# Optimization experiments

Measured on AMD Instinct MI355X. Metric: run time of the kernel, lower is better.

## Reference

```python
import jax, jax.numpy as jnp
import numpy as np

D_K = 128
SCALER = np.sqrt(D_K).astype(np.float32)

def setup_inputs() -> dict:
    key = jax.random.key(0)
    kq, kk, kv = jax.random.split(key, 3)
    B, L, D = 16, 2048, D_K
    q = jax.random.normal(kq, (B, L, D), dtype=jnp.float32)
    k = jax.random.normal(kk, (B, L, D), dtype=jnp.float32)
    v = jax.random.normal(kv, (B, L, D), dtype=jnp.float32)
    return {"q": q, "k": k, "v": v}

def reference(q, k, v):
    # score[b, i, j] = q[b, i, :] . k[b, j, :] / sqrt(d_k)
    score = jnp.einsum('bid,bjd->bij', q, k) / SCALER
    attn = jax.nn.softmax(score, axis=-1)
    # output[b, i, :] = sum_j attn[b, i, j] * v[b, j, :]
    return jnp.einsum('bij,bjd->bid', attn, v)
```

## Files before the change

kernel.cpp:

```cpp
#include <hip/hip_runtime.h>
#include <stdint.h>


typedef short bf16x8 __attribute__((ext_vector_type(8)));
typedef float f32x4 __attribute__((ext_vector_type(4)));
typedef float f32x16 __attribute__((ext_vector_type(16)));
typedef unsigned int u32;
typedef unsigned short u16;

#define L_SEQ  2048
#define D_HEAD 128
#define TSZ    8388608u
#define W_PART (2u * TSZ)
#define W_LSUM (W_PART + 512u * 32768u)
#define WS_NEED (W_LSUM + 512u * 128u * 4u)

__device__ __forceinline__ unsigned pk2(float lo, float hi) {
    union { float f; unsigned u; } a, b;
    a.f = lo; b.f = hi;
    return __builtin_amdgcn_perm(b.u + 0x8000u, a.u + 0x8000u, 0x07060302u);
}
__device__ __forceinline__ float ex2(float x) { return __builtin_amdgcn_exp2f(x); }
__device__ __forceinline__ float bflo(unsigned w) {
    union { unsigned u; float f; } v; v.u = w << 16; return v.f;
}
__device__ __forceinline__ float bfhi(unsigned w) {
    union { unsigned u; float f; } v; v.u = w & 0xffff0000u; return v.f;
}
__device__ __forceinline__ u32 cvtpk(float lo, float hi) {
    u32 d;
    asm("v_cvt_pk_bf16_f32 %0, %1, %2" : "=v"(d) : "v"(lo), "v"(hi));
    return d;
}
__device__ __forceinline__ void plswap(u32& a, u32& b) {
    asm volatile("v_permlane32_swap_b32 %0, %1" : "+v"(a), "+v"(b));
}
__device__ __forceinline__ void gl_lds16(const u16* g, u16* l) {
    __builtin_amdgcn_global_load_lds(
        (const __attribute__((address_space(1))) u32*)g,
        (__attribute__((address_space(3))) u32*)l, 16, 0, 0);
}

__global__ __launch_bounds__(256, 4)
void prepass(const float* __restrict__ K, const float* __restrict__ V,
             u16* __restrict__ kb, u16* __restrict__ vt) {
    const int id = blockIdx.x, t = threadIdx.x;
    if (id < 512) {
        const float* src = K + (size_t)id * 64 * 128;
        u16*        dst = kb + (size_t)id * 64 * 128;
        const int r = t >> 2;
        #pragma unroll
        for (int i = 0; i < 4; ++i) {
            int gp = (t & 3) * 4 + i;
            const float* s = src + r * 128 + gp * 8;
            float4 x0 = *(const float4*)s, x1 = *(const float4*)(s + 4);
            uint4 w;
            w.x = pk2(x0.x, x0.y); w.y = pk2(x0.z, x0.w);
            w.z = pk2(x1.x, x1.y); w.w = pk2(x1.z, x1.w);
            *(uint4*)(dst + (gp * 64 + r) * 8) = w;
        }
    } else {
        __shared__ __align__(16) u16 vl[128 * 72];
        const int bid = id - 512;
        const float* src = V + (size_t)bid * 64 * 128;
        const int vcc = t & 31, vgk = t >> 5;
        union { float4 v; float f[4]; } vr[8];
        const float* vp = src + (size_t)(vgk * 8) * 128 + vcc * 4;
        #pragma unroll
        for (int r = 0; r < 8; ++r) vr[r].v = *(const float4*)(vp + (size_t)r * 128);
        #pragma unroll
        for (int dd = 0; dd < 4; ++dd) {
            uint4 w;
            w.x = pk2(vr[0].f[dd], vr[1].f[dd]);
            w.y = pk2(vr[2].f[dd], vr[3].f[dd]);
            w.z = pk2(vr[4].f[dd], vr[5].f[dd]);
            w.w = pk2(vr[6].f[dd], vr[7].f[dd]);
            *(uint4*)(&vl[(vcc * 4 + dd) * 72 + vgk * 8]) = w;
        }
        __syncthreads();
        u16* dst = vt + (size_t)bid * 8192;
        #pragma unroll
        for (int i = 0; i < 4; ++i) {
            int c = i * 256 + t;
            int gv = c >> 7, d = c & 127;
            uint4 w = *(const uint4*)(&vl[d * 72 + gv * 8]);
            *(uint4*)(dst + (size_t)c * 8) = w;
        }
    }
}

__global__ __launch_bounds__(256, 2)
void attnR(const float* __restrict__ Qg, const u16* __restrict__ kb,
           const u16* __restrict__ vt, u16* __restrict__ part,
           float* __restrict__ lsum) {
    __shared__ __align__(16) char smem[32768];
    const int tid = threadIdx.x;
    const int qs = tid >> 6, lane = tid & 63;
    const int q32 = lane & 31, hi = lane >> 5;
    const int bid = blockIdx.x;
    const int kvh = bid >> 8, p = bid & 255;
    const int b = p & 15, qblk = p >> 4;
    const int nt = 16;

    const float* Qp = Qg + (size_t)b * L_SEQ * D_HEAD;
    const u16*   Kp = kb + (size_t)b * L_SEQ * D_HEAD + (size_t)kvh * 16 * 8192;
    const u16*   Vp = vt + (size_t)b * 32 * 8192 + (size_t)kvh * 16 * 8192;
    u16* Kl = (u16*)smem;
    u16* Vl = (u16*)(smem + 16384);
    const int so = qs * 2048 + lane * 8;

    #pragma unroll
    for (int i = 0; i < 4; ++i) {
        gl_lds16(Kp + so + i * 512, Kl + so + i * 512);
        gl_lds16(Vp + so + i * 512, Vl + so + i * 512);
    }

    const float QS = 1.4426950408889634f / 11.313708498984761f;
    bf16x8 qf[8];
    {
        const float* qrow = Qp + (size_t)(qblk * 128 + qs * 32 + q32) * 128 + hi * 8;
        #pragma unroll
        for (int s8 = 0; s8 < 8; ++s8) {
            float4 x0 = *(const float4*)(qrow + s8 * 16);
            float4 x1 = *(const float4*)(qrow + s8 * 16 + 4);
            union { u32 u[4]; bf16x8 v; } tt;
            tt.u[0] = pk2(x0.x * QS, x0.y * QS);
            tt.u[1] = pk2(x0.z * QS, x0.w * QS);
            tt.u[2] = pk2(x1.x * QS, x1.y * QS);
            tt.u[3] = pk2(x1.z * QS, x1.w * QS);
            qf[s8] = tt.v;
        }
    }

    f32x16 acc[4];
    #pragma unroll
    for (int dt = 0; dt < 4; ++dt)
        acc[dt] = (f32x16){0.f,0.f,0.f,0.f,0.f,0.f,0.f,0.f,
                           0.f,0.f,0.f,0.f,0.f,0.f,0.f,0.f};
    float lrun = 0.f;

    __syncthreads();

    for (int it = 0; it < nt; ++it) {
        f32x16 st0 = (f32x16){0.f,0.f,0.f,0.f,0.f,0.f,0.f,0.f,
                              0.f,0.f,0.f,0.f,0.f,0.f,0.f,0.f};
        f32x16 st1 = st0;
        const u16* Kbase = Kl + hi * 512 + q32 * 8;
        __builtin_amdgcn_s_setprio(1);
        #pragma unroll
        for (int s8 = 0; s8 < 8; ++s8) {
            bf16x8 a0 = *(const bf16x8*)(Kbase + s8 * 1024);
            bf16x8 a1 = *(const bf16x8*)(Kbase + s8 * 1024 + 256);
            st0 = __builtin_amdgcn_mfma_f32_32x32x16_bf16(a0, qf[s8], st0, 0, 0, 0);
            st1 = __builtin_amdgcn_mfma_f32_32x32x16_bf16(a1, qf[s8], st1, 0, 0, 0);
        }
        __builtin_amdgcn_s_setprio(0);
        __syncthreads();

        if (it + 1 < nt) {
            const u16* kg = Kp + (size_t)(it + 1) * 8192 + so;
            #pragma unroll
            for (int i = 0; i < 4; ++i) gl_lds16(kg + i * 512, Kl + so + i * 512);
        }

        bf16x8 pf[4];
        #pragma unroll
        for (int v = 0; v < 2; ++v) {
            float pp[16];
            #pragma unroll
            for (int e = 0; e < 16; ++e) {
                float sv = (v == 0) ? st0[e] : st1[e];
                pp[e] = ex2(sv);
                lrun += pp[e];
            }
            u32 wa0 = cvtpk(pp[0], pp[1]),  wb0 = cvtpk(pp[4], pp[5]);
            u32 wa1 = cvtpk(pp[2], pp[3]),  wb1 = cvtpk(pp[6], pp[7]);
            plswap(wa0, wb0); plswap(wa1, wb1);
            u32 wc0 = cvtpk(pp[8], pp[9]),  wd0 = cvtpk(pp[12], pp[13]);
            u32 wc1 = cvtpk(pp[10], pp[11]), wd1 = cvtpk(pp[14], pp[15]);
            plswap(wc0, wd0); plswap(wc1, wd1);
            union { u32 u[4]; bf16x8 x; } t0u, t1u;
            t0u.u[0] = wa0; t0u.u[1] = wa1; t0u.u[2] = wb0; t0u.u[3] = wb1;
            t1u.u[0] = wc0; t1u.u[1] = wc1; t1u.u[2] = wd0; t1u.u[3] = wd1;
            pf[v * 2]     = t0u.x;
            pf[v * 2 + 1] = t1u.x;
        }

        const u16* Vbase = Vl + hi * 1024 + q32 * 8;
        __builtin_amdgcn_s_setprio(1);
        #pragma unroll
        for (int dt = 0; dt < 4; ++dt) {
            #pragma unroll
            for (int ks = 0; ks < 4; ++ks) {
                bf16x8 av = *(const bf16x8*)(Vbase + ks * 2048 + dt * 256);
                acc[dt] = __builtin_amdgcn_mfma_f32_32x32x16_bf16(av, pf[ks], acc[dt], 0, 0, 0);
            }
        }
        __builtin_amdgcn_s_setprio(0);
        __syncthreads();

        if (it + 1 < nt) {
            const u16* vg = Vp + (size_t)(it + 1) * 8192 + so;
            #pragma unroll
            for (int i = 0; i < 4; ++i) gl_lds16(vg + i * 512, Vl + so + i * 512);
        }
    }

    float l = lrun + __shfl_xor(lrun, 32);
    uint2* pw = (uint2*)(part + (size_t)bid * 16384);
    #pragma unroll
    for (int dt = 0; dt < 4; ++dt) {
        f32x16 o = acc[dt];
        #pragma unroll
        for (int jj = 0; jj < 4; ++jj) {
            uint2 w;
            w.x = pk2(o[jj * 4 + 0], o[jj * 4 + 1]);
            w.y = pk2(o[jj * 4 + 2], o[jj * 4 + 3]);
            pw[(((qs * 4 + dt) * 4 + jj) << 6) + lane] = w;
        }
    }
    if (lane < 32)
        lsum[(size_t)bid * 128 + qs * 32 + lane] = l;
}

__global__ __launch_bounds__(256, 2)
void combineR(const u16* __restrict__ part, const float* __restrict__ lsum,
              float* __restrict__ Og) {
    __shared__ float inv[128];
    __shared__ __align__(16) float Ol[64 * 132];
    const int t = threadIdx.x, p = blockIdx.x;
    const int b = p & 15, qblk = p >> 4;
    if (t < 128) {
        float l = lsum[(size_t)p * 128 + t] + lsum[(size_t)(256 + p) * 128 + t];
        inv[t] = 1.0f / l;
    }
    const uint2* S0 = (const uint2*)(part + (size_t)p * 16384);
    const uint2* S1 = (const uint2*)(part + (size_t)(256 + p) * 16384);
    __syncthreads();
    #pragma unroll
    for (int h = 0; h < 2; ++h) {
        #pragma unroll
        for (int i = 0; i < 8; ++i) {
            int slot = i * 256 + t;
            int qs_l = slot >> 10;
            int dt   = (slot >> 8) & 3;
            int jj   = (slot >> 6) & 3;
            int lane = slot & 63;
            int hi = lane >> 5, q32 = lane & 31;
            int qs = h * 2 + qs_l;
            int row_l = qs_l * 32 + q32;
            int d0 = dt * 32 + hi * 4 + jj * 8;
            size_t idx = (size_t)(((qs * 4 + dt) * 4 + jj) << 6) + lane;
            uint2 w0 = S0[idx], w1 = S1[idx];
            float iv = inv[h * 64 + row_l];
            float4 o;
            o.x = (bflo(w0.x) + bflo(w1.x)) * iv;
            o.y = (bfhi(w0.x) + bfhi(w1.x)) * iv;
            o.z = (bflo(w0.y) + bflo(w1.y)) * iv;
            o.w = (bfhi(w0.y) + bfhi(w1.y)) * iv;
            *(float4*)(&Ol[row_l * 132 + d0]) = o;
        }
        __syncthreads();
        #pragma unroll
        for (int i = 0; i < 8; ++i) {
            int slot = i * 256 + t;
            int row = slot >> 5, c4 = slot & 31;
            float4 val = *(const float4*)(&Ol[row * 132 + c4 * 4]);
            size_t q = (size_t)b * L_SEQ + qblk * 128 + h * 64 + row;
            *(float4*)(Og + q * D_HEAD + c4 * 4) = val;
        }
        __syncthreads();
    }
}

extern "C" void kernel_launch(void* const* d_in, const int* in_sizes, int n_in,
                              void* d_out, int out_size, void* d_ws, size_t ws_size,
                              hipStream_t stream) {
    const float* q = (const float*)d_in[0];
    const float* k = (const float*)d_in[1];
    const float* v = (const float*)d_in[2];
    float* out = (float*)d_out;
    u16* kb = (u16*)d_ws;
    u16* vt = (u16*)((char*)d_ws + TSZ);
    u16* part = (u16*)((char*)d_ws + W_PART);
    float* ls = (float*)((char*)d_ws + W_LSUM);
    prepass<<<dim3(1024), dim3(256), 0, stream>>>(k, v, kb, vt);
    attnR<<<dim3(512), dim3(256), 0, stream>>>(q, kb, vt, part, ls);
    combineR<<<dim3(256), dim3(256), 0, stream>>>(part, ls, out);
}
```

Baseline: 134.1 us.

## Fuse split-KV combine into attention kernel via last-arriver atomic flag

Removes the separate combine kernel. Each attention block stores its partial output and row sums, then bumps a per-tile counter; the second block to arrive reads its partner's partial and writes the normalized output directly from its own fp32 accumulators. This saves a kernel launch and a full round trip of partials, and the arriving block's own half stays in fp32 rather than being rounded to bf16. In exchange it relies on agent-scope atomics for cross-block visibility, writes output with uncoalesced per-lane float4 stores without LDS staging, and also drops the s_setprio hints around the MFMA loops.

Result: slower. 146.8 us (+9.5%).

```diff
diff --git a/kernel.cpp b/kernel.cpp
--- a/kernel.cpp
+++ b/kernel.cpp
@@ -3,9 +3,9 @@
 
 
 typedef short bf16x8 __attribute__((ext_vector_type(8)));
-typedef float f32x4 __attribute__((ext_vector_type(4)));
 typedef float f32x16 __attribute__((ext_vector_type(16)));
 typedef unsigned int u32;
+typedef unsigned long long u64;
 typedef unsigned short u16;
 
 #define L_SEQ  2048
@@ -13,7 +13,7 @@
 #define TSZ    8388608u
 #define W_PART (2u * TSZ)
 #define W_LSUM (W_PART + 512u * 32768u)
-#define WS_NEED (W_LSUM + 512u * 128u * 4u)
+#define W_FLAG (W_LSUM + 512u * 128u * 4u)
 
 __device__ __forceinline__ unsigned pk2(float lo, float hi) {
     union { float f; unsigned u; } a, b;
@@ -43,8 +43,10 @@
 
 __global__ __launch_bounds__(256, 4)
 void prepass(const float* __restrict__ K, const float* __restrict__ V,
-             u16* __restrict__ kb, u16* __restrict__ vt) {
+             u16* __restrict__ kb, u16* __restrict__ vt, int* __restrict__ flag) {
     const int id = blockIdx.x, t = threadIdx.x;
+    if (id == 0)
+        __hip_atomic_store(&flag[t], 0, __ATOMIC_RELAXED, __HIP_MEMORY_SCOPE_AGENT);
     if (id < 512) {
         const float* src = K + (size_t)id * 64 * 128;
         u16*        dst = kb + (size_t)id * 64 * 128;
@@ -92,8 +94,10 @@
 __global__ __launch_bounds__(256, 2)
 void attnR(const float* __restrict__ Qg, const u16* __restrict__ kb,
            const u16* __restrict__ vt, u16* __restrict__ part,
-           float* __restrict__ lsum) {
+           float* __restrict__ lsum, int* __restrict__ flag,
+           float* __restrict__ Og) {
     __shared__ __align__(16) char smem[32768];
+    __shared__ int role;
     const int tid = threadIdx.x;
     const int qs = tid >> 6, lane = tid & 63;
     const int q32 = lane & 31, hi = lane >> 5;
@@ -146,7 +150,6 @@
                               0.f,0.f,0.f,0.f,0.f,0.f,0.f,0.f};
         f32x16 st1 = st0;
         const u16* Kbase = Kl + hi * 512 + q32 * 8;
-        __builtin_amdgcn_s_setprio(1);
         #pragma unroll
         for (int s8 = 0; s8 < 8; ++s8) {
             bf16x8 a0 = *(const bf16x8*)(Kbase + s8 * 1024);
@@ -154,7 +157,6 @@
             st0 = __builtin_amdgcn_mfma_f32_32x32x16_bf16(a0, qf[s8], st0, 0, 0, 0);
             st1 = __builtin_amdgcn_mfma_f32_32x32x16_bf16(a1, qf[s8], st1, 0, 0, 0);
         }
-        __builtin_amdgcn_s_setprio(0);
         __syncthreads();
 
         if (it + 1 < nt) {
@@ -187,7 +189,6 @@
         }
 
         const u16* Vbase = Vl + hi * 1024 + q32 * 8;
-        __builtin_amdgcn_s_setprio(1);
         #pragma unroll
         for (int dt = 0; dt < 4; ++dt) {
             #pragma unroll
@@ -196,7 +197,6 @@
                 acc[dt] = __builtin_amdgcn_mfma_f32_32x32x16_bf16(av, pf[ks], acc[dt], 0, 0, 0);
             }
         }
-        __builtin_amdgcn_s_setprio(0);
         __syncthreads();
 
         if (it + 1 < nt) {
@@ -207,69 +207,49 @@
     }
 
     float l = lrun + __shfl_xor(lrun, 32);
-    uint2* pw = (uint2*)(part + (size_t)bid * 16384);
+    u64* pw = (u64*)(part + (size_t)bid * 16384);
     #pragma unroll
     for (int dt = 0; dt < 4; ++dt) {
-        f32x16 o = acc[dt];
         #pragma unroll
         for (int jj = 0; jj < 4; ++jj) {
-            uint2 w;
-            w.x = pk2(o[jj * 4 + 0], o[jj * 4 + 1]);
-            w.y = pk2(o[jj * 4 + 2], o[jj * 4 + 3]);
-            pw[(((qs * 4 + dt) * 4 + jj) << 6) + lane] = w;
+            u32 wx = pk2(acc[dt][jj * 4 + 0], acc[dt][jj * 4 + 1]);
+            u32 wy = pk2(acc[dt][jj * 4 + 2], acc[dt][jj * 4 + 3]);
+            u64 v = ((u64)wy << 32) | wx;
+            __hip_atomic_store(&pw[(((qs * 4 + dt) * 4 + jj) << 6) + lane], v,
+                               __ATOMIC_RELAXED, __HIP_MEMORY_SCOPE_AGENT);
         }
     }
     if (lane < 32)
-        lsum[(size_t)bid * 128 + qs * 32 + lane] = l;
-}
-
-__global__ __launch_bounds__(256, 2)
-void combineR(const u16* __restrict__ part, const float* __restrict__ lsum,
-              float* __restrict__ Og) {
-    __shared__ float inv[128];
-    __shared__ __align__(16) float Ol[64 * 132];
-    const int t = threadIdx.x, p = blockIdx.x;
-    const int b = p & 15, qblk = p >> 4;
-    if (t < 128) {
-        float l = lsum[(size_t)p * 128 + t] + lsum[(size_t)(256 + p) * 128 + t];
-        inv[t] = 1.0f / l;
-    }
-    const uint2* S0 = (const uint2*)(part + (size_t)p * 16384);
-    const uint2* S1 = (const uint2*)(part + (size_t)(256 + p) * 16384);
+        __hip_atomic_store(&lsum[(size_t)bid * 128 + qs * 32 + lane], l,
+                           __ATOMIC_RELAXED, __HIP_MEMORY_SCOPE_AGENT);
+
     __syncthreads();
-    #pragma unroll
-    for (int h = 0; h < 2; ++h) {
-        #pragma unroll
-        for (int i = 0; i < 8; ++i) {
-            int slot = i * 256 + t;
-            int qs_l = slot >> 10;
-            int dt   = (slot >> 8) & 3;
-            int jj   = (slot >> 6) & 3;
-            int lane = slot & 63;
-            int hi = lane >> 5, q32 = lane & 31;
-            int qs = h * 2 + qs_l;
-            int row_l = qs_l * 32 + q32;
-            int d0 = dt * 32 + hi * 4 + jj * 8;
-            size_t idx = (size_t)(((qs * 4 + dt) * 4 + jj) << 6) + lane;
-            uint2 w0 = S0[idx], w1 = S1[idx];
-            float iv = inv[h * 64 + row_l];
+    if (tid == 0)
+        role = __hip_atomic_fetch_add(&flag[p], 1, __ATOMIC_ACQ_REL,
+                                      __HIP_MEMORY_SCOPE_AGENT);
+    __syncthreads();
+    if (role == 0) return;
+
+    const int pbid = bid ^ 256;
+    const u64* pr = (const u64*)(part + (size_t)pbid * 16384);
+    float lp = __hip_atomic_load(&lsum[(size_t)pbid * 128 + qs * 32 + q32],
+                                 __ATOMIC_RELAXED, __HIP_MEMORY_SCOPE_AGENT);
+    float iv = 1.0f / (l + lp);
+    float* orow = Og + ((size_t)b * L_SEQ + qblk * 128 + qs * 32 + q32) * 128;
+    #pragma unroll
+    for (int dt = 0; dt < 4; ++dt) {
+        #pragma unroll
+        for (int jj = 0; jj < 4; ++jj) {
+            u64 v = __hip_atomic_load(&pr[(((qs * 4 + dt) * 4 + jj) << 6) + lane],
+                                      __ATOMIC_RELAXED, __HIP_MEMORY_SCOPE_AGENT);
+            u32 wx = (u32)v, wy = (u32)(v >> 32);
             float4 o;
-            o.x = (bflo(w0.x) + bflo(w1.x)) * iv;
-            o.y = (bfhi(w0.x) + bfhi(w1.x)) * iv;
-            o.z = (bflo(w0.y) + bflo(w1.y)) * iv;
-            o.w = (bfhi(w0.y) + bfhi(w1.y)) * iv;
-            *(float4*)(&Ol[row_l * 132 + d0]) = o;
-        }
-        __syncthreads();
-        #pragma unroll
-        for (int i = 0; i < 8; ++i) {
-            int slot = i * 256 + t;
-            int row = slot >> 5, c4 = slot & 31;
-            float4 val = *(const float4*)(&Ol[row * 132 + c4 * 4]);
-            size_t q = (size_t)b * L_SEQ + qblk * 128 + h * 64 + row;
-            *(float4*)(Og + q * D_HEAD + c4 * 4) = val;
-        }
-        __syncthreads();
+            o.x = (acc[dt][jj * 4 + 0] + bflo(wx)) * iv;
+            o.y = (acc[dt][jj * 4 + 1] + bfhi(wx)) * iv;
+            o.z = (acc[dt][jj * 4 + 2] + bflo(wy)) * iv;
+            o.w = (acc[dt][jj * 4 + 3] + bfhi(wy)) * iv;
+            *(float4*)(orow + dt * 32 + hi * 4 + jj * 8) = o;
+        }
     }
 }
 
@@ -284,7 +264,7 @@
     u16* vt = (u16*)((char*)d_ws + TSZ);
     u16* part = (u16*)((char*)d_ws + W_PART);
     float* ls = (float*)((char*)d_ws + W_LSUM);
-    prepass<<<dim3(1024), dim3(256), 0, stream>>>(k, v, kb, vt);
-    attnR<<<dim3(512), dim3(256), 0, stream>>>(q, kb, vt, part, ls);
-    combineR<<<dim3(256), dim3(256), 0, stream>>>(part, ls, out);
-}
+    int* flag = (int*)((char*)d_ws + W_FLAG);
+    prepass<<<dim3(1024), dim3(256), 0, stream>>>(k, v, kb, vt, flag);
+    attnR<<<dim3(512), dim3(256), 0, stream>>>(q, kb, vt, part, ls, flag, out);
+}
```
